# Optimization experiments

Hardware: AMD Instinct MI355X
Metric: run time of the kernel (lower is better)

## Reference

```python
import jax, jax.numpy as jnp
import numpy as np

NEG_SLOPE = 0.2  # PyG GATv2 default negative_slope


def _gru_last(x, W_ih, W_hh, b_ih, b_hh):
    """x: [B, T, Hin] -> final GRU hidden state [B, H] (torch nn.GRU equations)."""
    gx = x @ W_ih.T + b_ih  # [B, T, 3H], input gates precomputed
    H = W_hh.shape[1]

    def step(h, g):
        gh = h @ W_hh.T + b_hh
        xr, xz, xn = jnp.split(g, 3, axis=-1)
        hr, hz, hn = jnp.split(gh, 3, axis=-1)
        r = jax.nn.sigmoid(xr + hr)
        z = jax.nn.sigmoid(xz + hz)
        n = jnp.tanh(xn + r * hn)
        return (1.0 - z) * n + z * h, None

    h0 = jnp.zeros((x.shape[0], H), x.dtype)
    hT, _ = jax.lax.scan(step, h0, jnp.swapaxes(gx, 0, 1))
    return hT


def _conv(x, w, b, stride):
    y = jax.lax.conv_general_dilated(x, w, (stride, stride), 'SAME',
                                     dimension_numbers=('NCHW', 'OIHW', 'NCHW'))
    return jax.nn.relu(y + b[None, :, None, None])


def _forward(obs, phase, obs_map, edges, edges_feature, params):
    (W_nbrs, b_nbrs, W_ih, W_hh, b_ih, b_hh, Wl, Wr, att_a, gat_bias,
     conv1_w, conv1_b, conv2_w, conv2_b, Wc, bc, Wp, bp, Wh, bh,
     Wo, bo, Wa, ba) = params
    B, N = obs.shape[0], obs.shape[1]
    BN = B * N
    heads, C = att_a.shape

    # per-node obs embedding (MLP) + GRU over seq -> last hidden
    x = jax.nn.relu(obs.reshape(BN, obs.shape[2], obs.shape[3]) @ W_nbrs + b_nbrs)
    h = _gru_last(x, W_ih, W_hh, b_ih, b_hh)  # [BN, hidden]

    # flat_edges: offset each sample's node ids by b*N, concat along edge dim
    offsets = (jnp.arange(B) * N)[:, None, None]
    ei = (edges + offsets).transpose(1, 0, 2).reshape(2, -1)  # [2, B*E]
    loops = jnp.arange(BN)  # PyG GATv2 add_self_loops=True
    src = jnp.concatenate([ei[0], loops])
    dst = jnp.concatenate([ei[1], loops])

    # GATv2Conv (heads, concat=False): gather -> leakyrelu -> edge softmax -> scatter
    xl = (h @ Wl).reshape(BN, heads, C)
    xr = (h @ Wr).reshape(BN, heads, C)
    e = jax.nn.leaky_relu(xl[src] + xr[dst], NEG_SLOPE)  # [Etot, heads, C]
    logits = jnp.einsum('ehc,hc->eh', e, att_a)          # [Etot, heads]
    m = jax.ops.segment_max(logits, dst, num_segments=BN)
    p = jnp.exp(logits - m[dst])
    s = jax.ops.segment_sum(p, dst, num_segments=BN)
    alpha = p / s[dst]                                    # [Etot, heads]
    node_out = jax.ops.segment_sum(xl[src] * alpha[..., None], dst, num_segments=BN)
    obs_gat = node_out.mean(axis=1) + gat_bias            # concat=False -> head mean

    source_idx = jnp.arange(B) * N  # ego intersection of each sample
    obs_gat = obs_gat[source_idx]   # [B, hidden]

    # CNNBase on map
    c = _conv(obs_map, conv1_w, conv1_b, 2)
    c = _conv(c, conv2_w, conv2_b, 2)
    target_emb = jax.nn.relu(c.reshape(B, -1) @ Wc + bc)

    # phase MLP, fusion MLP, dueling head
    phase_emb = jax.nn.relu(phase @ Wp + bp)
    fused = jnp.concatenate([obs_gat, target_emb, phase_emb], axis=1)
    hid = jax.nn.relu(fused @ Wh + bh)
    v = hid @ Wo + bo
    adv = hid @ Wa + ba
    out = v + (adv - adv.mean(axis=-1, keepdims=True))
    return out, alpha


def setup_inputs() -> dict:
    key = jax.random.key(0)
    B, N, T, Fo = 16, 1000, 16, 16      # batch, n_nodes, seq_len, obs_length+4
    H, heads, P, A, E = 128, 5, 8, 8, 4000
    Cm, HW = 4, 32
    ks = iter(jax.random.split(key, 40))

    def rn(shape, scale=0.05):
        return jax.random.normal(next(ks), shape, dtype=jnp.float32) * scale

    return dict(
        obs=rn((B, N, T, Fo), 1.0),
        phase=rn((B, P), 1.0),
        obs_map=rn((B, Cm, HW, HW), 1.0),
        edges=jax.random.randint(next(ks), (B, 2, E), 0, N),
        edges_feature=rn((B, E, 4), 1.0),
        W_nbrs=rn((Fo, H)), b_nbrs=jnp.zeros((H,), jnp.float32),
        W_ih=rn((3 * H, H)), W_hh=rn((3 * H, H)),
        b_ih=jnp.zeros((3 * H,), jnp.float32), b_hh=jnp.zeros((3 * H,), jnp.float32),
        Wl=rn((H, heads * H)), Wr=rn((H, heads * H)),
        att_a=rn((heads, H)), gat_bias=jnp.zeros((H,), jnp.float32),
        conv1_w=rn((32, Cm, 3, 3)), conv1_b=jnp.zeros((32,), jnp.float32),
        conv2_w=rn((64, 32, 3, 3)), conv2_b=jnp.zeros((64,), jnp.float32),
        Wc=rn((64 * (HW // 4) * (HW // 4), H)), bc=jnp.zeros((H,), jnp.float32),
        Wp=rn((P, P)), bp=jnp.zeros((P,), jnp.float32),
        Wh=rn((2 * H + P, H)), bh=jnp.zeros((H,), jnp.float32),
        Wo=rn((H, 1)), bo=jnp.zeros((1,), jnp.float32),
        Wa=rn((H, A)), ba=jnp.zeros((A,), jnp.float32),
    )


def reference(obs, phase, obs_map, edges, edges_feature,
              W_nbrs, b_nbrs, W_ih, W_hh, b_ih, b_hh,
              Wl, Wr, att_a, gat_bias,
              conv1_w, conv1_b, conv2_w, conv2_b, Wc, bc,
              Wp, bp, Wh, bh, Wo, bo, Wa, ba):
    params = (W_nbrs, b_nbrs, W_ih, W_hh, b_ih, b_hh, Wl, Wr, att_a, gat_bias,
              conv1_w, conv1_b, conv2_w, conv2_b, Wc, bc, Wp, bp, Wh, bh,
              Wo, bo, Wa, ba)
    return _forward(obs, phase, obs_map, edges, edges_feature, params)
```

## Files before the change

kernel.cpp:

```cpp
#include <hip/hip_runtime.h>
#include <hip/hip_bf16.h>
#include <math.h>

#define B_    16
#define N_    1000
#define BN_   16000
#define T_    16
#define FO    16
#define H_    128
#define G3    384
#define HEADS 5
#define HC    640
#define E_    4000
#define EG    64000
#define ETOT  80000
#define P_    8
#define A_    8
#define NEG_SLOPE 0.2f

typedef __attribute__((ext_vector_type(8))) short bf16x8;
typedef __attribute__((ext_vector_type(4))) float f32x4;

__device__ __forceinline__ float bf2f(unsigned short u){ return __uint_as_float(((unsigned)u)<<16); }
__device__ __forceinline__ unsigned short f2bf(float x){
    unsigned u = __float_as_uint(x);
    unsigned r = (u + 0x7FFFu + ((u>>16)&1u)) >> 16;
    return (unsigned short)r;
}
__device__ __forceinline__ unsigned cvtpk(float lo, float hi){
    unsigned r;
    asm volatile("v_cvt_pk_bf16_f32 %0, %1, %2" : "=v"(r) : "v"(lo), "v"(hi));
    return r;
}
__device__ __forceinline__ float rcpf(float x){ return __builtin_amdgcn_rcpf(x); }

__global__ __launch_bounds__(256) void k_prep_c1(
        const float* __restrict__ Wih, const float* __restrict__ Whh,
        const float* __restrict__ Wl, const float* __restrict__ Wr,
        const float* __restrict__ Wn, const float* __restrict__ bn,
        unsigned short* __restrict__ Wihb, unsigned short* __restrict__ Whhb,
        unsigned short* __restrict__ WTb, unsigned short* __restrict__ WnTb,
        float* __restrict__ segsum, float* __restrict__ node_out,
        float* __restrict__ tacc,
        const float* __restrict__ im, const float* __restrict__ w1,
        const float* __restrict__ b1, float* __restrict__ c1out){
    __shared__ float sW[32*4*9];
    int t = threadIdx.x;
    if(blockIdx.x < 640){
        int i = blockIdx.x*256 + t;
        if(i < G3*H_){ Wihb[i] = f2bf(Wih[i]); Whhb[i] = f2bf(Whh[i]); }
        if(i < 2*HC*H_){
            int c = i >> 7, k = i & 127;
            float v = (c < HC) ? Wl[(size_t)k*HC + c] : Wr[(size_t)k*HC + (c-HC)];
            WTb[i] = f2bf(v);
        }
        if(i < H_*32){
            int c = i >> 5, k = i & 31;
            WnTb[i] = (k < FO) ? f2bf(Wn[k*H_ + c])
                     : (k == FO ? f2bf(bn[c]) : (unsigned short)0);
        }
        if(i < BN_*HEADS) segsum[i] = 0.0f;
        if(i < B_*HC) node_out[i] = 0.0f;
        if(i < B_*H_) tacc[i] = 0.0f;
    } else {
        for(int i=t;i<32*4*9;i+=256) sW[i]=w1[i];
        __syncthreads();
        int idx = (blockIdx.x-640)*256 + t;
        int ox = idx & 15, oy = (idx>>4)&15, oc = (idx>>8)&31, b = idx>>13;
        float acc = b1[oc];
        for(int ic=0;ic<4;ic++){
            const float* ip = &im[(size_t)((b*4+ic)*32)*32];
            const float* wp = &sW[(oc*4+ic)*9];
            #pragma unroll
            for(int ky=0;ky<3;ky++){
                int iy = oy*2+ky; if(iy>=32) continue;
                #pragma unroll
                for(int kx=0;kx<3;kx++){
                    int ix = ox*2+kx; if(ix>=32) continue;
                    acc = fmaf(ip[iy*32+ix], wp[ky*3+kx], acc);
                }
            }
        }
        c1out[idx] = fmaxf(acc, 0.f);
    }
}

__global__ __launch_bounds__(512,2) void k_gruf(const float* __restrict__ obs,
        const unsigned short* __restrict__ WnTb,
        const unsigned short* __restrict__ Wihb, const float* __restrict__ bih,
        const unsigned short* __restrict__ Whhb, const float* __restrict__ bhh,
        const unsigned short* __restrict__ WTb,
        unsigned short* __restrict__ xl, unsigned short* __restrict__ xr){
    __shared__ unsigned short sX[2*8192];
    __shared__ unsigned short sH[2*8192];
    int t = threadIdx.x;
    int w = t>>6, lane = t&63, lq = lane>>4, lm = lane&15;

    bf16x8 wfi[3][4], wfh[3][4];
    #pragma unroll
    for(int i=0;i<3;i++){
        int row = (8*i + w)*16 + lm;
        #pragma unroll
        for(int kt=0;kt<4;kt++){
            wfi[i][kt] = *(const bf16x8*)&Wihb[row*H_ + kt*32 + lq*8];
            wfh[i][kt] = *(const bf16x8*)&Whhb[row*H_ + kt*32 + lq*8];
        }
    }
    bf16x8 wfn = *(const bf16x8*)&WnTb[(w*16+lm)*32 + lq*8];
    int cb = w*16 + lq*4;
    f32x4 b_r, b_z, bxn, bhn;
    { f32x4 t1=*(const f32x4*)&bih[cb],     t2=*(const f32x4*)&bhh[cb];     b_r=t1+t2; }
    { f32x4 t1=*(const f32x4*)&bih[128+cb], t2=*(const f32x4*)&bhh[128+cb]; b_z=t1+t2; }
    bxn = *(const f32x4*)&bih[256+cb];
    bhn = *(const f32x4*)&bhh[256+cb];

    int rd[4];
    #pragma unroll
    for(int kt=0;kt<4;kt++) rd[kt] = lm*128 + (((4*kt+lq)^(lm&7))<<3);
    const int wrt = lm*128 + (((2*w + (lq>>1))^(lm&7))<<3) + ((lq&1)<<2);

    int nodeBase = blockIdx.x*64;
    const float* obp0 = &obs[(size_t)(nodeBase + lm)*256 + lq*8];

    for(int i=t;i<4096;i+=512) ((unsigned*)sH)[i] = 0u;
    float ho[4][4] = {{0.f,0.f,0.f,0.f},{0.f,0.f,0.f,0.f},
                      {0.f,0.f,0.f,0.f},{0.f,0.f,0.f,0.f}};

    float4 oA[4], oB[4];
    if(lq < 2){
        #pragma unroll
        for(int g=0; g<4; g++){
            const float* q = obp0 + (size_t)g*16*256;
            oA[g] = *(const float4*)(q);    oB[g] = *(const float4*)(q+4);
        }
    }
    #pragma unroll
    for(int g=0; g<4; g++){
        bf16x8 ob = (bf16x8){0,0,0,0,0,0,0,0};
        if(lq < 2){
            union { uint4 u; bf16x8 v; } cv;
            cv.u = make_uint4(cvtpk(oA[g].x,oA[g].y), cvtpk(oA[g].z,oA[g].w),
                              cvtpk(oB[g].x,oB[g].y), cvtpk(oB[g].z,oB[g].w));
            ob = cv.v;
        } else if(lq == 2){
            ob[0] = (short)0x3F80;
        }
        f32x4 xa = (f32x4){0.f,0.f,0.f,0.f};
        xa = __builtin_amdgcn_mfma_f32_16x16x32_bf16(wfn, ob, xa, 0,0,0);
        unsigned u0 = cvtpk(fmaxf(xa[0],0.f), fmaxf(xa[1],0.f));
        unsigned u1 = cvtpk(fmaxf(xa[2],0.f), fmaxf(xa[3],0.f));
        *(uint2*)&sX[g*2048 + wrt] = make_uint2(u0,u1);
    }
    __syncthreads();

    int p = 0;
    #pragma unroll 1
    for(int s=0; s<T_; s++){
        if(s < T_-1 && lq < 2){
            #pragma unroll
            for(int g=0; g<4; g++){
                const float* q = obp0 + (size_t)g*16*256 + (s+1)*16;
                oA[g] = *(const float4*)(q);    oB[g] = *(const float4*)(q+4);
            }
        }
        #pragma unroll
        for(int g=0; g<4; g++){
            int base = p*8192 + g*2048;
            bf16x8 xb[4], hb[4];
            #pragma unroll
            for(int kt=0;kt<4;kt++){
                xb[kt] = *(const bf16x8*)&sX[base + rd[kt]];
                hb[kt] = *(const bf16x8*)&sH[base + rd[kt]];
            }
            f32x4 ar = b_r, az = b_z, axi = bxn, ahh = bhn;
            #pragma unroll
            for(int kt=0;kt<4;kt++){
                ar  = __builtin_amdgcn_mfma_f32_16x16x32_bf16(wfi[0][kt], xb[kt], ar, 0,0,0);
                az  = __builtin_amdgcn_mfma_f32_16x16x32_bf16(wfi[1][kt], xb[kt], az, 0,0,0);
                axi = __builtin_amdgcn_mfma_f32_16x16x32_bf16(wfi[2][kt], xb[kt], axi, 0,0,0);
                ar  = __builtin_amdgcn_mfma_f32_16x16x32_bf16(wfh[0][kt], hb[kt], ar, 0,0,0);
                az  = __builtin_amdgcn_mfma_f32_16x16x32_bf16(wfh[1][kt], hb[kt], az, 0,0,0);
                ahh = __builtin_amdgcn_mfma_f32_16x16x32_bf16(wfh[2][kt], hb[kt], ahh, 0,0,0);
            }
            #pragma unroll
            for(int v=0;v<4;v++){
                float er = __expf(-ar[v]);
                float r  = rcpf(1.f + er);
                float ez = __expf(-az[v]);
                float z  = rcpf(1.f + ez);
                float xn = fmaf(r, ahh[v], axi[v]);
                float en = __expf(-2.f*xn);
                float nn = fmaf(2.f, rcpf(1.f + en), -1.f);
                ho[g][v] = nn + z*(ho[g][v] - nn);
            }
            unsigned u0 = cvtpk(ho[g][0], ho[g][1]);
            unsigned u1 = cvtpk(ho[g][2], ho[g][3]);
            *(uint2*)&sH[(p^1)*8192 + g*2048 + wrt] = make_uint2(u0,u1);
        }
        if(s < T_-1){
            #pragma unroll
            for(int g=0; g<4; g++){
                bf16x8 ob = (bf16x8){0,0,0,0,0,0,0,0};
                if(lq < 2){
                    union { uint4 u; bf16x8 v; } cv;
                    cv.u = make_uint4(cvtpk(oA[g].x,oA[g].y), cvtpk(oA[g].z,oA[g].w),
                                      cvtpk(oB[g].x,oB[g].y), cvtpk(oB[g].z,oB[g].w));
                    ob = cv.v;
                } else if(lq == 2){
                    ob[0] = (short)0x3F80;
                }
                f32x4 xa = (f32x4){0.f,0.f,0.f,0.f};
                xa = __builtin_amdgcn_mfma_f32_16x16x32_bf16(wfn, ob, xa, 0,0,0);
                unsigned u0 = cvtpk(fmaxf(xa[0],0.f), fmaxf(xa[1],0.f));
                unsigned u1 = cvtpk(fmaxf(xa[2],0.f), fmaxf(xa[3],0.f));
                *(uint2*)&sX[(p^1)*8192 + g*2048 + wrt] = make_uint2(u0,u1);
            }
        }
        __syncthreads();
        p ^= 1;
    }

    bf16x8 wfA[4], wfB[4];
    {
        int row = w*16 + lm;
        #pragma unroll
        for(int kt=0;kt<4;kt++)
            wfA[kt] = *(const bf16x8*)&WTb[(size_t)row*H_ + kt*32 + lq*8];
    }
    bf16x8 hba[4][4];
    #pragma unroll
    for(int g=0;g<4;g++){
        #pragma unroll
        for(int kt=0;kt<4;kt++)
            hba[g][kt] = *(const bf16x8*)&sH[p*8192 + g*2048 + rd[kt]];
    }
    #pragma unroll 1
    for(int tt=0; tt<10; tt++){
        if(tt < 9){
            int row = (w + (tt+1)*8)*16 + lm;
            #pragma unroll
            for(int kt=0;kt<4;kt++)
                wfB[kt] = *(const bf16x8*)&WTb[(size_t)row*H_ + kt*32 + lq*8];
        }
        int tile = w + tt*8;
        #pragma unroll
        for(int g=0;g<4;g++){
            f32x4 acc = (f32x4){0.f,0.f,0.f,0.f};
            #pragma unroll
            for(int kt=0;kt<4;kt++)
                acc = __builtin_amdgcn_mfma_f32_16x16x32_bf16(wfA[kt], hba[g][kt], acc, 0,0,0);
            int node = nodeBase + g*16 + lm;
            int col = tile*16 + lq*4;
            ushort4 o;
            o.x=f2bf(acc[0]); o.y=f2bf(acc[1]); o.z=f2bf(acc[2]); o.w=f2bf(acc[3]);
            if(col < HC) *(ushort4*)&xl[(size_t)node*HC + col] = o;
            else         *(ushort4*)&xr[(size_t)node*HC + (col-HC)] = o;
        }
        #pragma unroll
        for(int kt=0;kt<4;kt++) wfA[kt] = wfB[kt];
    }
}

__global__ __launch_bounds__(256) void k_conv2(const float* __restrict__ c1,
        const float* __restrict__ w, const float* __restrict__ bias, float* __restrict__ outp){
    int idx = blockIdx.x*256 + threadIdx.x;
    if(idx >= 16*64*8*8) return;
    int ox = idx & 7, oy = (idx>>3)&7, oc = (idx>>6)&63, b = idx>>12;
    float acc = bias[oc];
    for(int ic=0;ic<32;ic++){
        const float* ip = &c1[(size_t)((b*32+ic)*16)*16];
        const float* wp = &w[(oc*32+ic)*9];
        #pragma unroll
        for(int ky=0;ky<3;ky++){
            int iy = oy*2+ky; if(iy>=16) continue;
            #pragma unroll
            for(int kx=0;kx<3;kx++){
                int ix = ox*2+kx; if(ix>=16) continue;
                acc = fmaf(ip[iy*16+ix], wp[ky*3+kx], acc);
            }
        }
    }
    outp[idx] = fmaxf(acc, 0.f);
}

__device__ __forceinline__ void edge_sd(int e, const int* __restrict__ edges, int* src, int* dst){
    if(e < EG){
        int b = e / E_, j = e - b*E_;
        *src = edges[(b*2+0)*E_ + j] + b*N_;
        *dst = edges[(b*2+1)*E_ + j] + b*N_;
    } else { *src = *dst = e - EG; }
}

__global__ __launch_bounds__(256) void k_logits_tb(const unsigned short* __restrict__ xl,
        const unsigned short* __restrict__ xr, const int* __restrict__ edges,
        const float* __restrict__ atta, float* __restrict__ pbuf,
        float* __restrict__ segsum,
        const float* __restrict__ c2, const float* __restrict__ Wc,
        float* __restrict__ tacc){
    __shared__ float sC[128];
    int t = threadIdx.x;
    if(blockIdx.x < 5000){
        int lb = (blockIdx.x & 7)*625 + (blockIdx.x >> 3);
        int lane = t & 63, w = t >> 6;
        float am[8], a4[8];
        #pragma unroll
        for(int j=0;j<8;j++) am[j] = atta[lane*8+j];
        #pragma unroll
        for(int j=0;j<8;j++) a4[j] = (lane<16) ? atta[512+lane*8+j] : 0.f;

        int e0 = lb*16 + w*4;
        int srcs[4], dsts[4];
        #pragma unroll
        for(int i=0;i<4;i++) edge_sd(e0+i, edges, &srcs[i], &dsts[i]);
        #pragma unroll
        for(int i=0;i<4;i++){
            const unsigned short* xls = &xl[(size_t)srcs[i]*HC];
            const unsigned short* xrd = &xr[(size_t)dsts[i]*HC];
            uint4 ul = *(const uint4*)&xls[lane*8];
            uint4 ur = *(const uint4*)&xrd[lane*8];
            uint4 tl = make_uint4(0,0,0,0), tr = make_uint4(0,0,0,0);
            if(lane < 16){
                tl = *(const uint4*)&xls[512+lane*8];
                tr = *(const uint4*)&xrd[512+lane*8];
            }
            float pm = 0.f, p4 = 0.f;
            {
                unsigned pl[4] = {ul.x,ul.y,ul.z,ul.w};
                unsigned pr[4] = {ur.x,ur.y,ur.z,ur.w};
                #pragma unroll
                for(int q=0;q<4;q++){
                    float s0 = bf2f((unsigned short)(pl[q]&0xFFFFu)) + bf2f((unsigned short)(pr[q]&0xFFFFu));
                    float s1 = bf2f((unsigned short)(pl[q]>>16))     + bf2f((unsigned short)(pr[q]>>16));
                    s0 = s0 > 0.f ? s0 : NEG_SLOPE*s0;
                    s1 = s1 > 0.f ? s1 : NEG_SLOPE*s1;
                    pm = fmaf(s0, am[2*q],   pm);
                    pm = fmaf(s1, am[2*q+1], pm);
                }
            }
            {
                unsigned ql[4] = {tl.x,tl.y,tl.z,tl.w};
                unsigned qr[4] = {tr.x,tr.y,tr.z,tr.w};
                #pragma unroll
                for(int q=0;q<4;q++){
                    float s0 = bf2f((unsigned short)(ql[q]&0xFFFFu)) + bf2f((unsigned short)(qr[q]&0xFFFFu));
                    float s1 = bf2f((unsigned short)(ql[q]>>16))     + bf2f((unsigned short)(qr[q]>>16));
                    s0 = s0 > 0.f ? s0 : NEG_SLOPE*s0;
                    s1 = s1 > 0.f ? s1 : NEG_SLOPE*s1;
                    p4 = fmaf(s0, a4[2*q],   p4);
                    p4 = fmaf(s1, a4[2*q+1], p4);
                }
            }
            #pragma unroll
            for(int off=1; off<16; off<<=1){
                pm += __shfl_xor(pm, off);
                p4 += __shfl_xor(p4, off);
            }
            if((lane & 15) == 0){
                int hh = lane >> 4;
                float p = __expf(pm);
                pbuf[(size_t)(e0+i)*HEADS + hh] = p;
                atomicAdd(&segsum[dsts[i]*HEADS + hh], p);
            }
            if(lane == 8){
                float p = __expf(p4);
                pbuf[(size_t)(e0+i)*HEADS + 4] = p;
                atomicAdd(&segsum[dsts[i]*HEADS + 4], p);
            }
        }
    } else {
        int bb = blockIdx.x - 5000;
        int b = bb >> 5, ks = bb & 31;
        int k0 = ks*128;
        if(t < 128) sC[t] = c2[(size_t)b*4096 + k0 + t];
        __syncthreads();
        int j = t & 127, sub = t >> 7;
        const float* wp = &Wc[(size_t)(k0 + sub*64)*H_ + j];
        const float* cp = &sC[sub*64];
        float a0=0.f, a1=0.f, a2=0.f, a3=0.f;
        #pragma unroll
        for(int kk=0; kk<64; kk+=4){
            a0 = fmaf(cp[kk+0], wp[(size_t)(kk+0)*H_], a0);
            a1 = fmaf(cp[kk+1], wp[(size_t)(kk+1)*H_], a1);
            a2 = fmaf(cp[kk+2], wp[(size_t)(kk+2)*H_], a2);
            a3 = fmaf(cp[kk+3], wp[(size_t)(kk+3)*H_], a3);
        }
        atomicAdd(&tacc[b*H_+j], (a0+a1)+(a2+a3));
    }
}

__global__ void k_alpha(const float* __restrict__ pbuf, const float* __restrict__ segsum,
                        const int* __restrict__ edges, const unsigned short* __restrict__ xl,
                        float* __restrict__ out_alpha, float* __restrict__ node_out){
    int idx = blockIdx.x*256 + threadIdx.x;
    int lane = threadIdx.x & 63;
    bool valid = idx < ETOT*HEADS;
    int e = 0, hh = 0, src = 0, dst = 0;
    float a = 0.f;
    bool ego = false;
    if(valid){
        e = idx / HEADS; hh = idx - e*HEADS;
        edge_sd(e, edges, &src, &dst);
        a = pbuf[idx] / segsum[dst*HEADS + hh];
        out_alpha[idx] = a;
        ego = (dst % N_) == 0;
    }
    unsigned long long m = __ballot(ego);
    while(m){
        int l = __ffsll((unsigned long long)m) - 1;
        m &= (m - 1);
        float aa = __shfl(a, l);
        int ss = __shfl(src, l), dd = __shfl(dst, l), hq = __shfl(hh, l);
        int b = dd / N_;
        unsigned u = *(const unsigned*)&xl[(size_t)ss*HC + hq*H_ + lane*2];
        float* no = &node_out[b*HC + hq*H_ + lane*2];
        atomicAdd(no,     aa * bf2f((unsigned short)(u & 0xFFFFu)));
        atomicAdd(no + 1, aa * bf2f((unsigned short)(u >> 16)));
    }
}

__global__ __launch_bounds__(256) void k_head(const float* __restrict__ node_out,
        const float* __restrict__ gat_bias, const float* __restrict__ tacc,
        const float* __restrict__ bc, const float* __restrict__ phase,
        const float* __restrict__ Wp, const float* __restrict__ bp,
        const float* __restrict__ Wh, const float* __restrict__ bh,
        const float* __restrict__ Wo, const float* __restrict__ bo,
        const float* __restrict__ Wa, const float* __restrict__ ba,
        float* __restrict__ out){
    __shared__ float sF[268];
    __shared__ float sHid[128];
    int t = threadIdx.x;
    int b = blockIdx.x;
    if(t < 128){
        float s=0.f;
        #pragma unroll
        for(int hh=0;hh<HEADS;hh++) s += node_out[b*HC + hh*H_ + t];
        sF[t] = s*(1.0f/HEADS) + gat_bias[t];
    } else {
        int c = t - 128;
        sF[128+c] = fmaxf(tacc[b*H_ + c] + bc[c], 0.f);
    }
    if(t < P_){
        float s=bp[t];
        #pragma unroll
        for(int q=0;q<P_;q++) s = fmaf(phase[b*P_+q], Wp[q*P_+t], s);
        sF[256+t] = fmaxf(s, 0.f);
    }
    __syncthreads();
    if(t < 128){
        float s=bh[t];
        for(int k=0;k<2*H_+P_;k++) s = fmaf(sF[k], Wh[k*H_+t], s);
        sHid[t]=fmaxf(s,0.f);
    }
    __syncthreads();
    if(t < A_){
        float v=bo[0], ad=ba[t];
        for(int k=0;k<H_;k++){ float hv=sHid[k]; v = fmaf(hv,Wo[k],v); ad = fmaf(hv,Wa[k*A_+t],ad); }
        float m = ad;
        m += __shfl_xor(m,1); m += __shfl_xor(m,2); m += __shfl_xor(m,4);
        m *= 0.125f;
        out[b*A_+t] = v + ad - m;
    }
}

extern "C" void kernel_launch(void* const* d_in, const int* in_sizes, int n_in,
                              void* d_out, int out_size, void* d_ws, size_t ws_size,
                              hipStream_t stream) {
    (void)in_sizes; (void)n_in; (void)out_size; (void)ws_size;
    const float* obs      = (const float*)d_in[0];
    const float* phase    = (const float*)d_in[1];
    const float* obs_map  = (const float*)d_in[2];
    const int*   edges    = (const int*)  d_in[3];
    const float* W_nbrs   = (const float*)d_in[5];
    const float* b_nbrs   = (const float*)d_in[6];
    const float* W_ih     = (const float*)d_in[7];
    const float* W_hh     = (const float*)d_in[8];
    const float* b_ih     = (const float*)d_in[9];
    const float* b_hh     = (const float*)d_in[10];
    const float* Wl       = (const float*)d_in[11];
    const float* Wr       = (const float*)d_in[12];
    const float* att_a    = (const float*)d_in[13];
    const float* gat_bias = (const float*)d_in[14];
    const float* conv1_w  = (const float*)d_in[15];
    const float* conv1_b  = (const float*)d_in[16];
    const float* conv2_w  = (const float*)d_in[17];
    const float* conv2_b  = (const float*)d_in[18];
    const float* Wc       = (const float*)d_in[19];
    const float* bc       = (const float*)d_in[20];
    const float* Wp       = (const float*)d_in[21];
    const float* bp       = (const float*)d_in[22];
    const float* Wh       = (const float*)d_in[23];
    const float* bh       = (const float*)d_in[24];
    const float* Wo       = (const float*)d_in[25];
    const float* bo       = (const float*)d_in[26];
    const float* Wa       = (const float*)d_in[27];
    const float* ba       = (const float*)d_in[28];

    float* out = (float*)d_out;
    float* w   = (float*)d_ws;

    size_t off = 0;
    unsigned short* xl   = (unsigned short*)(w + off); off += (size_t)BN_*HC/2;
    unsigned short* xr   = (unsigned short*)(w + off); off += (size_t)BN_*HC/2;
    float* pbuf   = w + off; off += (size_t)ETOT*HEADS;
    float* segsum = w + off; off += (size_t)BN_*HEADS;
    float* nodeo  = w + off; off += (size_t)B_*HC;
    float* c1     = w + off; off += (size_t)16*32*16*16;
    float* c2     = w + off; off += (size_t)16*64*8*8;
    float* tacc   = w + off; off += (size_t)B_*H_;
    unsigned short* Wihb = (unsigned short*)(w + off); off += (size_t)H_*G3/2;
    unsigned short* Whhb = (unsigned short*)(w + off); off += (size_t)H_*G3/2;
    unsigned short* WTb  = (unsigned short*)(w + off); off += (size_t)2*HC*H_/2;
    unsigned short* WnTb = (unsigned short*)(w + off); off += (size_t)H_*32/2;

    k_prep_c1<<<640 + 512, 256, 0, stream>>>(W_ih, W_hh, Wl, Wr, W_nbrs, b_nbrs,
                                             Wihb, Whhb, WTb, WnTb,
                                             segsum, nodeo, tacc,
                                             obs_map, conv1_w, conv1_b, c1);

    k_gruf<<<250, 512, 0, stream>>>(obs, WnTb, Wihb, b_ih, Whhb, b_hh, WTb, xl, xr);

    k_conv2<<<(16*64*8*8)/256, 256, 0, stream>>>(c1, conv2_w, conv2_b, c2);

    k_logits_tb<<<5000 + 512, 256, 0, stream>>>(xl, xr, edges, att_a, pbuf, segsum,
                                                c2, Wc, tacc);

    k_alpha<<<(ETOT*HEADS+255)/256, 256, 0, stream>>>(pbuf, segsum, edges, xl, out+128, nodeo);

    k_head<<<B_, 256, 0, stream>>>(nodeo, gat_bias, tacc, bc, phase,
                                   Wp, bp, Wh, bh, Wo, bo, Wa, ba, out);
}
```

Before: 166.8 us.

## Fold conv2 into logits kernel and conv-to-hidden matmul into alpha kernel

Removes the standalone conv2 launch by running it as extra tail blocks of the logits kernel, and moves the conv-flatten matmul (Wc accumulation) from the logits kernel into the alpha kernel's tail blocks. This cuts one kernel launch and keeps the small map-branch work overlapped with the graph kernels. The map branch now spans two dependent kernels, so conv2 has to finish within the logits launch before Wc consumes its output.

```diff
diff --git a/kernel.cpp b/kernel.cpp
--- a/kernel.cpp
+++ b/kernel.cpp
@@ -261,28 +261,6 @@
     }
 }
 
-__global__ __launch_bounds__(256) void k_conv2(const float* __restrict__ c1,
-        const float* __restrict__ w, const float* __restrict__ bias, float* __restrict__ outp){
-    int idx = blockIdx.x*256 + threadIdx.x;
-    if(idx >= 16*64*8*8) return;
-    int ox = idx & 7, oy = (idx>>3)&7, oc = (idx>>6)&63, b = idx>>12;
-    float acc = bias[oc];
-    for(int ic=0;ic<32;ic++){
-        const float* ip = &c1[(size_t)((b*32+ic)*16)*16];
-        const float* wp = &w[(oc*32+ic)*9];
-        #pragma unroll
-        for(int ky=0;ky<3;ky++){
-            int iy = oy*2+ky; if(iy>=16) continue;
-            #pragma unroll
-            for(int kx=0;kx<3;kx++){
-                int ix = ox*2+kx; if(ix>=16) continue;
-                acc = fmaf(ip[iy*16+ix], wp[ky*3+kx], acc);
-            }
-        }
-    }
-    outp[idx] = fmaxf(acc, 0.f);
-}
-
 __device__ __forceinline__ void edge_sd(int e, const int* __restrict__ edges, int* src, int* dst){
     if(e < EG){
         int b = e / E_, j = e - b*E_;
@@ -291,13 +269,12 @@
     } else { *src = *dst = e - EG; }
 }
 
-__global__ __launch_bounds__(256) void k_logits_tb(const unsigned short* __restrict__ xl,
+__global__ __launch_bounds__(256) void k_logits_c2(const unsigned short* __restrict__ xl,
         const unsigned short* __restrict__ xr, const int* __restrict__ edges,
         const float* __restrict__ atta, float* __restrict__ pbuf,
         float* __restrict__ segsum,
-        const float* __restrict__ c2, const float* __restrict__ Wc,
-        float* __restrict__ tacc){
-    __shared__ float sC[128];
+        const float* __restrict__ c1, const float* __restrict__ w2,
+        const float* __restrict__ b2, float* __restrict__ c2out){
     int t = threadIdx.x;
     if(blockIdx.x < 5000){
         int lb = (blockIdx.x & 7)*625 + (blockIdx.x >> 3);
@@ -368,7 +345,62 @@
             }
         }
     } else {
-        int bb = blockIdx.x - 5000;
+        int idx = (blockIdx.x-5000)*256 + t;
+        int ox = idx & 7, oy = (idx>>3)&7, oc = (idx>>6)&63, b = idx>>12;
+        float acc = b2[oc];
+        for(int ic=0;ic<32;ic++){
+            const float* ip = &c1[(size_t)((b*32+ic)*16)*16];
+            const float* wp = &w2[(oc*32+ic)*9];
+            #pragma unroll
+            for(int ky=0;ky<3;ky++){
+                int iy = oy*2+ky; if(iy>=16) continue;
+                #pragma unroll
+                for(int kx=0;kx<3;kx++){
+                    int ix = ox*2+kx; if(ix>=16) continue;
+                    acc = fmaf(ip[iy*16+ix], wp[ky*3+kx], acc);
+                }
+            }
+        }
+        c2out[idx] = fmaxf(acc, 0.f);
+    }
+}
+
+__global__ __launch_bounds__(256) void k_alpha_tb(const float* __restrict__ pbuf,
+        const float* __restrict__ segsum, const int* __restrict__ edges,
+        const unsigned short* __restrict__ xl,
+        float* __restrict__ out_alpha, float* __restrict__ node_out,
+        const float* __restrict__ c2, const float* __restrict__ Wc,
+        float* __restrict__ tacc){
+    __shared__ float sC[128];
+    int t = threadIdx.x;
+    if(blockIdx.x < 1563){
+        int idx = blockIdx.x*256 + t;
+        int lane = t & 63;
+        bool valid = idx < ETOT*HEADS;
+        int e = 0, hh = 0, src = 0, dst = 0;
+        float a = 0.f;
+        bool ego = false;
+        if(valid){
+            e = idx / HEADS; hh = idx - e*HEADS;
+            edge_sd(e, edges, &src, &dst);
+            a = pbuf[idx] / segsum[dst*HEADS + hh];
+            out_alpha[idx] = a;
+            ego = (dst % N_) == 0;
+        }
+        unsigned long long m = __ballot(ego);
+        while(m){
+            int l = __ffsll((unsigned long long)m) - 1;
+            m &= (m - 1);
+            float aa = __shfl(a, l);
+            int ss = __shfl(src, l), dd = __shfl(dst, l), hq = __shfl(hh, l);
+            int b = dd / N_;
+            unsigned u = *(const unsigned*)&xl[(size_t)ss*HC + hq*H_ + lane*2];
+            float* no = &node_out[b*HC + hq*H_ + lane*2];
+            atomicAdd(no,     aa * bf2f((unsigned short)(u & 0xFFFFu)));
+            atomicAdd(no + 1, aa * bf2f((unsigned short)(u >> 16)));
+        }
+    } else {
+        int bb = blockIdx.x - 1563;
         int b = bb >> 5, ks = bb & 31;
         int k0 = ks*128;
         if(t < 128) sC[t] = c2[(size_t)b*4096 + k0 + t];
@@ -385,36 +417,6 @@
             a3 = fmaf(cp[kk+3], wp[(size_t)(kk+3)*H_], a3);
         }
         atomicAdd(&tacc[b*H_+j], (a0+a1)+(a2+a3));
-    }
-}
-
-__global__ void k_alpha(const float* __restrict__ pbuf, const float* __restrict__ segsum,
-                        const int* __restrict__ edges, const unsigned short* __restrict__ xl,
-                        float* __restrict__ out_alpha, float* __restrict__ node_out){
-    int idx = blockIdx.x*256 + threadIdx.x;
-    int lane = threadIdx.x & 63;
-    bool valid = idx < ETOT*HEADS;
-    int e = 0, hh = 0, src = 0, dst = 0;
-    float a = 0.f;
-    bool ego = false;
-    if(valid){
-        e = idx / HEADS; hh = idx - e*HEADS;
-        edge_sd(e, edges, &src, &dst);
-        a = pbuf[idx] / segsum[dst*HEADS + hh];
-        out_alpha[idx] = a;
-        ego = (dst % N_) == 0;
-    }
-    unsigned long long m = __ballot(ego);
-    while(m){
-        int l = __ffsll((unsigned long long)m) - 1;
-        m &= (m - 1);
-        float aa = __shfl(a, l);
-        int ss = __shfl(src, l), dd = __shfl(dst, l), hq = __shfl(hh, l);
-        int b = dd / N_;
-        unsigned u = *(const unsigned*)&xl[(size_t)ss*HC + hq*H_ + lane*2];
-        float* no = &node_out[b*HC + hq*H_ + lane*2];
-        atomicAdd(no,     aa * bf2f((unsigned short)(u & 0xFFFFu)));
-        atomicAdd(no + 1, aa * bf2f((unsigned short)(u >> 16)));
     }
 }
 
@@ -519,12 +521,11 @@
 
     k_gruf<<<250, 512, 0, stream>>>(obs, WnTb, Wihb, b_ih, Whhb, b_hh, WTb, xl, xr);
 
-    k_conv2<<<(16*64*8*8)/256, 256, 0, stream>>>(c1, conv2_w, conv2_b, c2);
-
-    k_logits_tb<<<5000 + 512, 256, 0, stream>>>(xl, xr, edges, att_a, pbuf, segsum,
-                                                c2, Wc, tacc);
-
-    k_alpha<<<(ETOT*HEADS+255)/256, 256, 0, stream>>>(pbuf, segsum, edges, xl, out+128, nodeo);
+    k_logits_c2<<<5000 + 256, 256, 0, stream>>>(xl, xr, edges, att_a, pbuf, segsum,
+                                                c1, conv2_w, conv2_b, c2);
+
+    k_alpha_tb<<<1563 + 512, 256, 0, stream>>>(pbuf, segsum, edges, xl, out+128, nodeo,
+                                               c2, Wc, tacc);
 
     k_head<<<B_, 256, 0, stream>>>(nodeo, gat_bias, tacc, bc, phase,
                                    Wp, bp, Wh, bh, Wo, bo, Wa, ba, out);
```

Measured after the change: 170.8 us. +2.4%, slower.
